# Kernel tuning notes

Hardware: AMD Instinct MI355X
Metric: run time of the kernel (lower is better)

## Reference

```python
import jax, jax.numpy as jnp
import numpy as np

N, C = 16384, 1000
P, Q, EPS = 0.6, 1.5, 0.01

def setup_inputs() -> dict:
    key = jax.random.key(0)
    k1, k2, k3 = jax.random.split(key, 3)
    logits = jax.random.normal(k1, (N, C), dtype=jnp.float32)
    targets = jax.random.randint(k2, (N,), 0, C, dtype=jnp.int64)
    # long-tailed cumulative class counts (float buffer in the torch module)
    cum_counts = jax.random.randint(k3, (C,), 1, 100000).astype(jnp.float32)
    return {"logits": logits, "targets": targets, "cum_counts": cum_counts}

def reference(logits, targets, cum_counts):
    # Seesaw loss (eval mode: no count update), reduction='mean'.
    n = logits.shape[0]
    tgt_count = jnp.maximum(cum_counts[targets], 1.0)            # (N,)  clamped target-class count
    # Mitigation factor: (count_j / count_t + eps)^p where count_j < count_t (strict)
    ratio_c = cum_counts[None, :] / tgt_count[:, None]           # (N, C)
    mitigation = jnp.where(cum_counts[None, :] < tgt_count[:, None],
                           jnp.power(ratio_c + EPS, P), 1.0)
    # Compensation factor: (p_j / (p_t + eps))^q where p_j > p_t
    probs = jax.nn.softmax(logits, axis=1)                       # (N, C)
    tgt_prob = jnp.take_along_axis(probs, targets[:, None], axis=1)  # (N, 1)
    compensation = jnp.where(probs > tgt_prob,
                             jnp.power(probs / (tgt_prob + EPS), Q), 1.0)
    # j == target column is always weight 1 (loops skip it)
    onehot = jax.nn.one_hot(targets, logits.shape[1], dtype=bool)
    weights = jnp.where(onehot, 1.0, mitigation * compensation)  # (N, C)
    weighted_logits = logits + jnp.log(weights + EPS)
    logp = jax.nn.log_softmax(weighted_logits, axis=1)
    loss = -jnp.take_along_axis(logp, targets[:, None], axis=1)[:, 0]
    return jnp.mean(loss)
```

## Files before the change

kernel.cpp:

```cpp
#include <hip/hip_runtime.h>
#include <math.h>


#define SSL_N 16384
#define SSL_C 1000
#define SSL_C4 250
#define SSL_P 0.6f
#define SSL_Q 1.5f
#define SSL_EPS 0.01f
#define SSL_LOG1PE 0.00995033085f
#define WPB 4
#define NBLK (SSL_N / WPB)

__global__ __launch_bounds__(256) void seesaw_main(
    const float* __restrict__ logits,
    const int*   __restrict__ targets,
    const float* __restrict__ cum_counts,
    float*       __restrict__ partial)
{
    __shared__ float cc[1024];
    __shared__ float blk[WPB];

    const int lane = threadIdx.x & 63;
    const int wave = threadIdx.x >> 6;
    const int row  = blockIdx.x * WPB + wave;

    const int t = targets[row];

    const float* __restrict__ lrow = logits + (size_t)row * SSL_C;
    const float4* __restrict__ lrow4 = reinterpret_cast<const float4*>(lrow);

    float4 lv[4];
    #pragma unroll
    for (int k = 0; k < 4; ++k) {
        const int j4 = lane + 64 * k;
        lv[k] = (j4 < SSL_C4) ? lrow4[j4]
                              : make_float4(-INFINITY, -INFINITY, -INFINITY, -INFINITY);
    }

    const float lt = lrow[t];

    for (int i = threadIdx.x; i < 1024; i += 256)
        cc[i] = (i < SSL_C) ? cum_counts[i] : 1.0f;
    __syncthreads();

    const float ct = fmaxf(cc[t], 1.0f);

    float s1 = 0.0f;
    #pragma unroll
    for (int k = 0; k < 4; ++k) {
        s1 += __expf(lv[k].x);
        s1 += __expf(lv[k].y);
        s1 += __expf(lv[k].z);
        s1 += __expf(lv[k].w);
    }
    #pragma unroll
    for (int off = 32; off >= 1; off >>= 1)
        s1 += __shfl_xor(s1, off, 64);

    const float pt     = __expf(lt) / s1;
    const float QK     = SSL_Q * (__logf(s1) + __logf(pt + SSL_EPS));
    const float inv_ct = 1.0f / ct;

    float s = 0.0f;
    #pragma unroll
    for (int k = 0; k < 4; ++k) {
        const int j4 = lane + 64 * k;
        const float4 c4 = *reinterpret_cast<const float4*>(&cc[4 * j4]);
        const float lvv[4] = { lv[k].x, lv[k].y, lv[k].z, lv[k].w };
        const float ccv[4] = { c4.x, c4.y, c4.z, c4.w };
        #pragma unroll
        for (int c = 0; c < 4; ++c) {
            const float lm = (ccv[c] < ct)
                ? SSL_P * __logf(fmaf(ccv[c], inv_ct, SSL_EPS)) : 0.0f;
            const float lc = (lvv[c] > lt)
                ? fmaf(SSL_Q, lvv[c], -QK) : 0.0f;
            s += __expf(lvv[c] + lm + lc);
        }
    }
    #pragma unroll
    for (int off = 32; off >= 1; off >>= 1)
        s += __shfl_xor(s, off, 64);

    const float s2   = fmaf(SSL_EPS, s1, s);
    const float loss = __logf(s2) - lt - SSL_LOG1PE;

    if (lane == 0) blk[wave] = loss;
    __syncthreads();
    if (threadIdx.x == 0) {
        float a = 0.0f;
        #pragma unroll
        for (int w = 0; w < WPB; ++w) a += blk[w];
        partial[blockIdx.x] = a;
    }
}

__global__ __launch_bounds__(1024) void ssl_reduce(
    const float* __restrict__ partial, float* __restrict__ out)
{
    float s = 0.0f;
    for (int i = threadIdx.x; i < NBLK; i += 1024) s += partial[i];
    #pragma unroll
    for (int off = 32; off >= 1; off >>= 1) s += __shfl_xor(s, off, 64);
    __shared__ float ws[16];
    if ((threadIdx.x & 63) == 0) ws[threadIdx.x >> 6] = s;
    __syncthreads();
    if (threadIdx.x == 0) {
        float a = 0.0f;
        #pragma unroll
        for (int w = 0; w < 16; ++w) a += ws[w];
        out[0] = a * (1.0f / SSL_N);
    }
}

extern "C" void kernel_launch(void* const* d_in, const int* in_sizes, int n_in,
                              void* d_out, int out_size, void* d_ws, size_t ws_size,
                              hipStream_t stream) {
    const float* logits     = (const float*)d_in[0];
    const int*   targets    = (const int*)d_in[1];
    const float* cum_counts = (const float*)d_in[2];
    float* out     = (float*)d_out;
    float* partial = (float*)d_ws;

    seesaw_main<<<NBLK, 256, 0, stream>>>(logits, targets, cum_counts, partial);
    ssl_reduce<<<1, 1024, 0, stream>>>(partial, out);
}
```

Baseline: 102.4 us.

## Drop shared-memory staging and barriers; extract target logit by shuffle

Removes the shared-memory copy of cum_counts and both __syncthreads, loading counts directly into registers per lane as float4 alongside the logits. The target logit is now taken from registers with a wave shuffle instead of a separate global load. Each wave writes its own per-row loss, and the reduce kernel sums all 16384 partials with vectorized loads instead of per-block sums. This trades block synchronization and LDS traffic for more register use and a larger final reduction.

```diff
diff --git a/kernel.cpp b/kernel.cpp
--- a/kernel.cpp
+++ b/kernel.cpp
@@ -11,6 +11,7 @@
 #define SSL_LOG1PE 0.00995033085f
 #define WPB 4
 #define NBLK (SSL_N / WPB)
+#define NEG_INF (-INFINITY)
 
 __global__ __launch_bounds__(256) void seesaw_main(
     const float* __restrict__ logits,
@@ -18,33 +19,29 @@
     const float* __restrict__ cum_counts,
     float*       __restrict__ partial)
 {
-    __shared__ float cc[1024];
-    __shared__ float blk[WPB];
+    const int lane = threadIdx.x & 63;
+    const int gw   = blockIdx.x * WPB + (threadIdx.x >> 6);
 
-    const int lane = threadIdx.x & 63;
-    const int wave = threadIdx.x >> 6;
-    const int row  = blockIdx.x * WPB + wave;
+    const int t = targets[gw];
 
-    const int t = targets[row];
+    const float4* __restrict__ lrow4 =
+        reinterpret_cast<const float4*>(logits + (size_t)gw * SSL_C);
+    const float4* __restrict__ cc4p =
+        reinterpret_cast<const float4*>(cum_counts);
 
-    const float* __restrict__ lrow = logits + (size_t)row * SSL_C;
-    const float4* __restrict__ lrow4 = reinterpret_cast<const float4*>(lrow);
-
-    float4 lv[4];
+    float4 lv[4], cc[4];
     #pragma unroll
     for (int k = 0; k < 4; ++k) {
         const int j4 = lane + 64 * k;
-        lv[k] = (j4 < SSL_C4) ? lrow4[j4]
-                              : make_float4(-INFINITY, -INFINITY, -INFINITY, -INFINITY);
+        if (j4 < SSL_C4) {
+            lv[k] = lrow4[j4];
+            cc[k] = cc4p[j4];
+        } else {
+            lv[k] = make_float4(NEG_INF, NEG_INF, NEG_INF, NEG_INF);
+            cc[k] = make_float4(1.0f, 1.0f, 1.0f, 1.0f);
+        }
     }
-
-    const float lt = lrow[t];
-
-    for (int i = threadIdx.x; i < 1024; i += 256)
-        cc[i] = (i < SSL_C) ? cum_counts[i] : 1.0f;
-    __syncthreads();
-
-    const float ct = fmaxf(cc[t], 1.0f);
+    const float ct = fmaxf(cum_counts[t], 1.0f);
 
     float s1 = 0.0f;
     #pragma unroll
@@ -58,6 +55,14 @@
     for (int off = 32; off >= 1; off >>= 1)
         s1 += __shfl_xor(s1, off, 64);
 
+    const int kk = t >> 8;
+    const int cc_sel = t & 3;
+    const float4 sel4 = (kk == 0) ? lv[0] : (kk == 1) ? lv[1]
+                      : (kk == 2) ? lv[2] : lv[3];
+    const float selv = (cc_sel == 0) ? sel4.x : (cc_sel == 1) ? sel4.y
+                     : (cc_sel == 2) ? sel4.z : sel4.w;
+    const float lt = __shfl(selv, (t >> 2) & 63, 64);
+
     const float pt     = __expf(lt) / s1;
     const float QK     = SSL_Q * (__logf(s1) + __logf(pt + SSL_EPS));
     const float inv_ct = 1.0f / ct;
@@ -66,40 +71,39 @@
     #pragma unroll
     for (int k = 0; k < 4; ++k) {
         const int j4 = lane + 64 * k;
-        const float4 c4 = *reinterpret_cast<const float4*>(&cc[4 * j4]);
-        const float lvv[4] = { lv[k].x, lv[k].y, lv[k].z, lv[k].w };
-        const float ccv[4] = { c4.x, c4.y, c4.z, c4.w };
-        #pragma unroll
-        for (int c = 0; c < 4; ++c) {
-            const float lm = (ccv[c] < ct)
-                ? SSL_P * __logf(fmaf(ccv[c], inv_ct, SSL_EPS)) : 0.0f;
-            const float lc = (lvv[c] > lt)
-                ? fmaf(SSL_Q, lvv[c], -QK) : 0.0f;
-            s += __expf(lvv[c] + lm + lc);
+        if (j4 < SSL_C4) {
+            const float lvv[4] = { lv[k].x, lv[k].y, lv[k].z, lv[k].w };
+            const float ccv[4] = { cc[k].x, cc[k].y, cc[k].z, cc[k].w };
+            #pragma unroll
+            for (int c = 0; c < 4; ++c) {
+                const float lm = (ccv[c] < ct)
+                    ? SSL_P * __logf(fmaf(ccv[c], inv_ct, SSL_EPS)) : 0.0f;
+                const float lc = (lvv[c] > lt)
+                    ? fmaf(SSL_Q, lvv[c], -QK) : 0.0f;
+                s += __expf(lvv[c] + lm + lc);
+            }
         }
     }
     #pragma unroll
     for (int off = 32; off >= 1; off >>= 1)
         s += __shfl_xor(s, off, 64);
 
-    const float s2   = fmaf(SSL_EPS, s1, s);
-    const float loss = __logf(s2) - lt - SSL_LOG1PE;
+    const float s2 = fmaf(SSL_EPS, s1, s);
 
-    if (lane == 0) blk[wave] = loss;
-    __syncthreads();
-    if (threadIdx.x == 0) {
-        float a = 0.0f;
-        #pragma unroll
-        for (int w = 0; w < WPB; ++w) a += blk[w];
-        partial[blockIdx.x] = a;
-    }
+    if (lane == 0)
+        partial[gw] = __logf(s2) - lt - SSL_LOG1PE;
 }
 
 __global__ __launch_bounds__(1024) void ssl_reduce(
     const float* __restrict__ partial, float* __restrict__ out)
 {
+    const float4* __restrict__ p4 = reinterpret_cast<const float4*>(partial);
     float s = 0.0f;
-    for (int i = threadIdx.x; i < NBLK; i += 1024) s += partial[i];
+    #pragma unroll
+    for (int k = 0; k < 4; ++k) {
+        const float4 v = p4[threadIdx.x + 1024 * k];
+        s += (v.x + v.y) + (v.z + v.w);
+    }
     #pragma unroll
     for (int off = 32; off >= 1; off >>= 1) s += __shfl_xor(s, off, 64);
     __shared__ float ws[16];
```

New measurement: 127.4 us. +24.4%, slower.
